# Kernel optimization log

Measured on AMD Instinct MI355X. Metric: run time of the kernel, lower is better.

The kernel has to match this reference:

```python
import jax, jax.numpy as jnp
import numpy as np

NH = 32          # num_attention_heads
LAYER_ID = 3     # -> query_key_layer_scaling_coeff = 4.0
ROPE_BASE = 10000.0


def setup_inputs() -> dict:
    key = jax.random.key(0)
    k1, k2, k3, k4, k5 = jax.random.split(key, 5)
    S, B, H = 2048, 1, 4096
    hidden_states = jax.random.normal(k1, (S, B, H), dtype=jnp.float32)
    position_ids = jnp.broadcast_to(jnp.arange(S, dtype=jnp.int64)[None, :], (B, S))
    # causal mask: True means masked out (torch masked_fill semantics)
    mask = jnp.triu(jnp.ones((S, S), dtype=bool), k=1)[None, None, :, :]
    qkv_w = jax.random.normal(k2, (3 * H, H), dtype=jnp.float32) * 0.02
    qkv_b = jax.random.normal(k3, (3 * H,), dtype=jnp.float32) * 0.02
    dense_w = jax.random.normal(k4, (H, H), dtype=jnp.float32) * 0.02
    dense_b = jax.random.normal(k5, (H,), dtype=jnp.float32) * 0.02
    return {"hidden_states": hidden_states, "position_ids": position_ids, "mask": mask,
            "qkv_w": qkv_w, "qkv_b": qkv_b, "dense_w": dense_w, "dense_b": dense_b}


def _rotate_half(x):
    h = x.shape[-1] // 2
    return jnp.concatenate((-x[..., h:], x[..., :h]), axis=-1)


def reference(hidden_states, position_ids, mask, qkv_w, qkv_b, dense_w, dense_b):
    S, B, H = hidden_states.shape
    nh = NH
    hd = H // nh
    coeff = float(LAYER_ID + 1)

    # fused QKV projection: [S, B, 3H] -> [S, B, nh, 3*hd] -> split
    mixed = hidden_states @ qkv_w.T + qkv_b
    mixed = mixed.reshape(S, B, nh, 3 * hd)
    q, k, v = jnp.split(mixed, 3, axis=-1)  # each [S, B, nh, hd]

    # rotary embedding indexed by position_ids (transposed to [S, B])
    pos = position_ids.T  # [S, B]
    inv_freq = 1.0 / (ROPE_BASE ** (jnp.arange(0, hd, 2, dtype=jnp.float32) / hd))
    freqs = pos.astype(jnp.float32)[..., None] * inv_freq  # [S, B, hd/2]
    emb = jnp.concatenate((freqs, freqs), axis=-1)          # [S, B, hd]
    cos = jnp.cos(emb)[:, :, None, :]                       # [S, B, 1, hd]
    sin = jnp.sin(emb)[:, :, None, :]
    q = q * cos + _rotate_half(q) * sin
    k = k * cos + _rotate_half(k) * sin

    # scaled attention scores with per-layer coefficient
    q = q / (jnp.sqrt(jnp.float32(hd)) * coeff)
    scores = jnp.einsum('sbnh,tbnh->bnst', q, k)            # [B, nh, S, S]
    scores = jnp.where(mask, jnp.float32(-10000.0), scores)
    probs = jax.nn.softmax(scores.astype(jnp.float32) * coeff, axis=-1)
    probs = probs.astype(scores.dtype)

    context = jnp.einsum('bnst,tbnh->sbnh', probs, v).reshape(S, B, H)
    output = context @ dense_w.T + dense_b                  # [S, B, H]
    return output
```

## Files before the change

### kernel.cpp

```cpp
#include <hip/hip_runtime.h>
#include <hip/hip_bf16.h>
#include <cstdint>

#define SQ   2048
#define HIDD 4096
#define NH_  32
#define HD_  128

typedef __attribute__((ext_vector_type(8))) __bf16 bf16x8;
typedef __attribute__((ext_vector_type(4))) float  f32x4;

__device__ __forceinline__ unsigned short f2bf(float f) {
  union { float f; unsigned u; } v; v.f = f;
  return (unsigned short)((v.u + 0x7FFFu + ((v.u >> 16) & 1u)) >> 16);
}
__device__ __forceinline__ float bf2f(unsigned short u) {
  union { unsigned u; float f; } v; v.u = ((unsigned)u) << 16; return v.f;
}
__device__ __forceinline__ void gload16(const void* g, void* l) {
  __builtin_amdgcn_global_load_lds((const __attribute__((address_space(1))) void*)g,
                                   (__attribute__((address_space(3))) void*)l, 16, 0, 0);
}
#define BAR()   asm volatile("s_barrier" ::: "memory")
#define VMC(N)  asm volatile("s_waitcnt vmcnt(" #N ")" ::: "memory")

__global__ __launch_bounds__(256) void k_conv(const float* __restrict__ src,
                                              unsigned short* __restrict__ dst, int n4) {
  int i = blockIdx.x * blockDim.x + threadIdx.x;
  int stride = gridDim.x * blockDim.x;
  for (; i < n4; i += stride) {
    float4 f = ((const float4*)src)[i];
    ushort4 o;
    o.x = f2bf(f.x); o.y = f2bf(f.y); o.z = f2bf(f.z); o.w = f2bf(f.w);
    ((ushort4*)dst)[i] = o;
  }
}

template<int MODE, int BN_>
__global__ __launch_bounds__(256, 2)
void k_gemm3(const unsigned short* __restrict__ A, const unsigned short* __restrict__ B,
             const float* __restrict__ bias, float* __restrict__ outf,
             unsigned short* __restrict__ qb, unsigned short* __restrict__ kb,
             unsigned short* __restrict__ vb, int K) {
  constexpr int NS   = 4 + BN_ / 32;
  constexpr int NF   = BN_ / 64;
  constexpr int BUFB = 16384 + BN_ * 128;
  __shared__ __align__(16) char lds[2 * BUFB];
  const int t = threadIdx.x;
  const int lane = t & 63, wc = t >> 6;
  const int lr = lane & 15, lg = lane >> 4;
  const int gx = gridDim.x;
  const int nwg = gx * gridDim.y;
  const int id = blockIdx.y * gx + blockIdx.x;
  const int cpx = nwg >> 3;
  const int swz = (id & 7) * cpx + (id >> 3);
  const int bm = swz % gx, bn = swz / gx;

  const unsigned short* src[NS];
  int dst[NS];
#pragma unroll
  for (int j = 0; j < NS; ++j) {
    int o = j * 4096 + t * 16;
    dst[j] = o;
    if (o < 16384) {
      int row = o >> 7, colb = o & 127;
      src[j] = A + (size_t)(bm * 128 + row) * K + ((colb ^ ((row & 7) << 4)) >> 1);
    } else {
      int o2 = o - 16384;
      int row = o2 >> 7, colb = o2 & 127;
      src[j] = B + (size_t)(bn * BN_ + row) * K + ((colb ^ ((row & 7) << 4)) >> 1);
    }
  }

  f32x4 acc[8][NF] = {};
  const int nk = K >> 6;
  const int swA = (lr & 7) << 4;

#pragma unroll
  for (int j = 0; j < NS; ++j) gload16(src[j], lds + dst[j]);

  int c = 0;
  for (int kt = 0; kt < nk; ++kt) {
    char* const bufc = lds + c * BUFB;
    char* const bufn = lds + (c ^ 1) * BUFB;
    if (kt + 1 < nk) {
      const int koff = (kt + 1) * 64;
#pragma unroll
      for (int j = 0; j < NS; ++j) gload16(src[j] + koff, bufn + dst[j]);
      if constexpr (NS == 10) VMC(10); else VMC(8);
    } else {
      VMC(0);
    }
    BAR();

    bf16x8 bfr[NF][2];
#pragma unroll
    for (int n = 0; n < NF; ++n) {
      const char* base = bufc + 16384 + (wc * (BN_ / 4) + n * 16 + lr) * 128;
#pragma unroll
      for (int kk = 0; kk < 2; ++kk)
        bfr[n][kk] = *(const bf16x8*)(base + ((kk * 64 + lg * 16) ^ swA));
    }
    __builtin_amdgcn_s_setprio(1);
#pragma unroll
    for (int m = 0; m < 8; ++m) {
      const char* abase = bufc + (m * 16 + lr) * 128;
      bf16x8 a0 = *(const bf16x8*)(abase + ((lg * 16) ^ swA));
      bf16x8 a1 = *(const bf16x8*)(abase + ((64 + lg * 16) ^ swA));
#pragma unroll
      for (int n = 0; n < NF; ++n) {
        acc[m][n] = __builtin_amdgcn_mfma_f32_16x16x32_bf16(a0, bfr[n][0], acc[m][n], 0, 0, 0);
        acc[m][n] = __builtin_amdgcn_mfma_f32_16x16x32_bf16(a1, bfr[n][1], acc[m][n], 0, 0, 0);
      }
    }
    __builtin_amdgcn_s_setprio(0);
    BAR();
    c ^= 1;
  }

#pragma unroll
  for (int m = 0; m < 8; ++m) {
    int row0 = bm * 128 + m * 16 + lg * 4;
#pragma unroll
    for (int n = 0; n < NF; ++n) {
      int col = bn * BN_ + wc * (BN_ / 4) + n * 16 + lr;
      float bv = bias[col];
      if (MODE == 0) {
        int h = col / 384, rem = col - h * 384;
        int sel = rem >> 7, d = rem & 127;
        unsigned short* dstp = sel == 0 ? qb : (sel == 1 ? kb : vb);
#pragma unroll
        for (int r = 0; r < 4; ++r)
          dstp[((size_t)h * SQ + row0 + r) * HD_ + d] = f2bf(acc[m][n][r] + bv);
      } else {
#pragma unroll
        for (int r = 0; r < 4; ++r)
          outf[(size_t)(row0 + r) * HIDD + col] = acc[m][n][r] + bv;
      }
    }
  }
}

__global__ __launch_bounds__(256) void k_rope(unsigned short* __restrict__ q,
                                              unsigned short* __restrict__ k) {
  int idx = blockIdx.x * blockDim.x + threadIdx.x;
  int i = idx & 63;
  int s = (idx >> 6) & (SQ - 1);
  int h = idx >> 17;
  float inv = __expf(-(float)i * (9.210340371976184f / 64.0f));
  float f = (float)s * inv;
  float sn, cs;
  sincosf(f, &sn, &cs);
  size_t base = ((size_t)h * SQ + s) * HD_ + i;
  const float qs = 0.08838834764831845f;
  float q0 = bf2f(q[base]), q1 = bf2f(q[base + 64]);
  q[base]      = f2bf((q0 * cs - q1 * sn) * qs);
  q[base + 64] = f2bf((q1 * cs + q0 * sn) * qs);
  float k0 = bf2f(k[base]), k1 = bf2f(k[base + 64]);
  k[base]      = f2bf(k0 * cs - k1 * sn);
  k[base + 64] = f2bf(k1 * cs + k0 * sn);
}

__global__ __launch_bounds__(256) void k_trans(const unsigned short* __restrict__ v,
                                               unsigned short* __restrict__ vt) {
  __shared__ unsigned short tile[32][33];
  const int h = blockIdx.z;
  const int sb = blockIdx.x * 32, db = blockIdx.y * 32;
  const unsigned short* src = v + (size_t)h * SQ * HD_;
  unsigned short* dst = vt + (size_t)h * HD_ * SQ;
  for (int r = threadIdx.y; r < 32; r += 8)
    tile[r][threadIdx.x] = src[(size_t)(sb + r) * HD_ + db + threadIdx.x];
  __syncthreads();
  for (int r = threadIdx.y; r < 32; r += 8)
    dst[(size_t)(db + r) * SQ + sb + threadIdx.x] = tile[threadIdx.x][r];
}

__global__ __launch_bounds__(256)
void k_attn(const unsigned short* __restrict__ q, const unsigned short* __restrict__ k,
            const unsigned short* __restrict__ vt, unsigned short* __restrict__ ctx) {
  __shared__ __align__(16) unsigned short Ks[64 * 128];
  __shared__ __align__(16) unsigned short Vs[128 * 64];
  __shared__ __align__(16) unsigned short Ps[4][16 * 64];

  const int h = blockIdx.y;
  const int t = threadIdx.x;
  const int lane = t & 63, wv = t >> 6;
  const int lr = lane & 15, lg = lane >> 4;

  const unsigned short* Kg = k + (size_t)h * SQ * HD_;
  const unsigned short* Vg = vt + (size_t)h * HD_ * SQ;
  char* const kl = (char*)Ks;
  char* const vl = (char*)Vs;
  char* const pb = (char*)(Ps[wv]);

  for (int ph = 0; ph < 2; ++ph) {
    const int tph = (ph == 0) ? (int)blockIdx.x : 31 - (int)blockIdx.x;
    const int q0p = tph * 64;
    const int qrow = wv * 16 + lg * 4;

    const unsigned short* Q = q + ((size_t)h * SQ + q0p + wv * 16) * HD_;
    bf16x8 qf[4];
#pragma unroll
    for (int kk = 0; kk < 4; ++kk)
      qf[kk] = *(const bf16x8*)(Q + (size_t)lr * HD_ + kk * 32 + lg * 8);

    f32x4 ot[8] = {};
    float m_r[4], l_r[4];
#pragma unroll
    for (int r = 0; r < 4; ++r) { m_r[r] = -1e30f; l_r[r] = 0.f; }

    const int nkt = tph + 1;
    for (int kt = 0; kt < nkt; ++kt) {
      const int kv0 = kt * 64;
      __syncthreads();
#pragma unroll
      for (int it = 0; it < 4; ++it) {
        int o = it * 4096 + t * 16;
        int krow = o >> 8, kcb = o & 255;
        int kscb = kcb ^ ((krow & 7) << 4);
        gload16(Kg + (size_t)(kv0 + krow) * HD_ + (kscb >> 1), kl + o);
        int vrow = o >> 7, vcb = o & 127;
        int vscb = vcb ^ ((vrow & 7) << 4);
        gload16(Vg + (size_t)vrow * SQ + kv0 + (vscb >> 1), vl + o);
      }
      __syncthreads();

      f32x4 sc[4] = {};
#pragma unroll
      for (int ct = 0; ct < 4; ++ct) {
        int row = ct * 16 + lr;
        const char* kbase = kl + row * 256;
#pragma unroll
        for (int kk = 0; kk < 4; ++kk) {
          bf16x8 kf = *(const bf16x8*)(kbase + ((kk * 64 + lg * 16) ^ ((row & 7) << 4)));
          sc[ct] = __builtin_amdgcn_mfma_f32_16x16x32_bf16(qf[kk], kf, sc[ct], 0, 0, 0);
        }
      }

      if (kt == tph) {
#pragma unroll
        for (int ct = 0; ct < 4; ++ct) {
          int col = ct * 16 + lr;
#pragma unroll
          for (int r = 0; r < 4; ++r)
            if (col > qrow + r) sc[ct][r] = -1e30f;
        }
      }

      float tmax[4];
#pragma unroll
      for (int r = 0; r < 4; ++r)
        tmax[r] = fmaxf(fmaxf(sc[0][r], sc[1][r]), fmaxf(sc[2][r], sc[3][r]));
#pragma unroll
      for (int off = 1; off < 16; off <<= 1)
#pragma unroll
        for (int r = 0; r < 4; ++r) tmax[r] = fmaxf(tmax[r], __shfl_xor(tmax[r], off, 64));

      float scf[4];
#pragma unroll
      for (int r = 0; r < 4; ++r) {
        float mn = fmaxf(m_r[r], tmax[r]);
        scf[r] = __expf(m_r[r] - mn);
        m_r[r] = mn;
      }
      float pr[4][4], rsum[4];
#pragma unroll
      for (int r = 0; r < 4; ++r) rsum[r] = 0.f;
#pragma unroll
      for (int ct = 0; ct < 4; ++ct)
#pragma unroll
        for (int r = 0; r < 4; ++r) {
          pr[ct][r] = __expf(sc[ct][r] - m_r[r]);
          rsum[r] += pr[ct][r];
        }
#pragma unroll
      for (int off = 1; off < 16; off <<= 1)
#pragma unroll
        for (int r = 0; r < 4; ++r) rsum[r] += __shfl_xor(rsum[r], off, 64);
#pragma unroll
      for (int r = 0; r < 4; ++r) l_r[r] = l_r[r] * scf[r] + rsum[r];

#pragma unroll
      for (int dt = 0; dt < 8; ++dt)
#pragma unroll
        for (int r = 0; r < 4; ++r) ot[dt][r] *= scf[r];

#pragma unroll
      for (int ct = 0; ct < 4; ++ct)
#pragma unroll
        for (int r = 0; r < 4; ++r) {
          int row = lg * 4 + r;
          int byte = row * 128 + ((ct * 32 + lr * 2) ^ ((row & 7) << 4));
          *(unsigned short*)(pb + byte) = f2bf(pr[ct][r]);
        }
      bf16x8 pa[2];
#pragma unroll
      for (int k2 = 0; k2 < 2; ++k2)
        pa[k2] = *(const bf16x8*)(pb + lr * 128 + ((k2 * 64 + lg * 16) ^ ((lr & 7) << 4)));

#pragma unroll
      for (int dt = 0; dt < 8; ++dt) {
        int row = dt * 16 + lr;
        const char* vbase = vl + row * 128;
        bf16x8 vf0 = *(const bf16x8*)(vbase + ((lg * 16) ^ ((row & 7) << 4)));
        bf16x8 vf1 = *(const bf16x8*)(vbase + ((64 + lg * 16) ^ ((row & 7) << 4)));
        ot[dt] = __builtin_amdgcn_mfma_f32_16x16x32_bf16(pa[0], vf0, ot[dt], 0, 0, 0);
        ot[dt] = __builtin_amdgcn_mfma_f32_16x16x32_bf16(pa[1], vf1, ot[dt], 0, 0, 0);
      }
    }

    float inv[4];
#pragma unroll
    for (int r = 0; r < 4; ++r) inv[r] = 1.0f / l_r[r];
#pragma unroll
    for (int dt = 0; dt < 8; ++dt)
#pragma unroll
      for (int r = 0; r < 4; ++r)
        ctx[(size_t)(q0p + wv * 16 + lg * 4 + r) * HIDD + h * HD_ + dt * 16 + lr] =
            f2bf(ot[dt][r] * inv[r]);
  }
}

extern "C" void kernel_launch(void* const* d_in, const int* in_sizes, int n_in,
                              void* d_out, int out_size, void* d_ws, size_t ws_size,
                              hipStream_t stream) {
  const float* hidden  = (const float*)d_in[0];
  const float* qkv_w   = (const float*)d_in[3];
  const float* qkv_b   = (const float*)d_in[4];
  const float* dense_w = (const float*)d_in[5];
  const float* dense_b = (const float*)d_in[6];
  float* out = (float*)d_out;

  char* ws = (char*)d_ws;
  unsigned short* wbuf = (unsigned short*)ws;
  unsigned short* hidb = (unsigned short*)(ws + 100663296);
  unsigned short* vtb  = hidb;
  unsigned short* qb   = (unsigned short*)(ws + 117440512);
  unsigned short* kb   = (unsigned short*)(ws + 134217728);
  unsigned short* vb   = (unsigned short*)(ws + 150994944);
  unsigned short* ctx  = (unsigned short*)(ws + 167772160);
  if (ws_size < 184549376ull) return;

  k_conv<<<2048, 256, 0, stream>>>(hidden, hidb, 8388608 / 4);
  k_conv<<<4096, 256, 0, stream>>>(qkv_w, wbuf, 50331648 / 4);
  k_gemm3<0, 192><<<dim3(16, 64), 256, 0, stream>>>(hidb, wbuf, qkv_b, nullptr, qb, kb, vb, 4096);
  k_rope<<<16384, 256, 0, stream>>>(qb, kb);
  k_trans<<<dim3(64, 4, 32), dim3(32, 8), 0, stream>>>(vb, vtb);
  k_attn<<<dim3(16, 32), 256, 0, stream>>>(qb, kb, vtb, ctx);
  k_conv<<<2048, 256, 0, stream>>>(dense_w, wbuf, 16777216 / 4);
  k_gemm3<1, 128><<<dim3(16, 32), 256, 0, stream>>>(ctx, wbuf, dense_b, out, nullptr, nullptr, nullptr, 4096);
}
```

Baseline: 459.4 us.

## Add 128x256 K=32 double-buffered GEMM kernel for QKV projection

Adds a new GEMM kernel that uses 128x256 output tiles with a K-step of 32, a 2-stage LDS double buffer and occupancy hint 3, and uses it for the QKV projection in place of the previous 128x192 multi-stage kernel. Each wave computes a 128x64 slice, so every A fragment read from LDS is reused across four MFMAs. The intent is better operand reuse per LDS read and higher occupancy to hide memory latency. In exchange the pipeline is shallower (only one tile prefetched), there is a barrier every 32-wide K step, and the epilogue still writes scattered bf16 stores.

```diff
diff --git a/kernel.cpp b/kernel.cpp
--- a/kernel.cpp
+++ b/kernel.cpp
@@ -33,6 +33,102 @@
     ushort4 o;
     o.x = f2bf(f.x); o.y = f2bf(f.y); o.z = f2bf(f.z); o.w = f2bf(f.w);
     ((ushort4*)dst)[i] = o;
+  }
+}
+
+template<int MODE>
+__global__ __launch_bounds__(256, 3)
+void k_gemm4(const unsigned short* __restrict__ A, const unsigned short* __restrict__ B,
+             const float* __restrict__ bias, float* __restrict__ outf,
+             unsigned short* __restrict__ qb, unsigned short* __restrict__ kb,
+             unsigned short* __restrict__ vb, int K) {
+  __shared__ __align__(16) char lds[2 * 24576];
+  const int t = threadIdx.x;
+  const int lane = t & 63, wc = t >> 6;
+  const int lr = lane & 15, lg = lane >> 4;
+  const int gx = gridDim.x;
+  const int nwg = gx * gridDim.y;
+  const int id = blockIdx.y * gx + blockIdx.x;
+  const int cpx = nwg >> 3;
+  const int swz = (id & 7) * cpx + (id >> 3);
+  const int bm = swz % gx, bn = swz / gx;
+
+  const unsigned short* src[6];
+  int dst[6];
+#pragma unroll
+  for (int j = 0; j < 6; ++j) {
+    int o = j * 4096 + t * 16;
+    dst[j] = o;
+    if (o < 8192) {
+      int row = o >> 6, colb = o & 63;
+      src[j] = A + (size_t)(bm * 128 + row) * K + ((colb ^ ((row & 3) << 4)) >> 1);
+    } else {
+      int o2 = o - 8192;
+      int row = o2 >> 6, colb = o2 & 63;
+      src[j] = B + (size_t)(bn * 256 + row) * K + ((colb ^ ((row & 3) << 4)) >> 1);
+    }
+  }
+
+  f32x4 acc[8][4] = {};
+  const int nk = K >> 5;
+  const int swF = (lr & 3) << 4;
+
+#pragma unroll
+  for (int j = 0; j < 6; ++j) gload16(src[j], lds + dst[j]);
+
+  int c = 0;
+  for (int kt = 0; kt < nk; ++kt) {
+    char* const bufc = lds + c * 24576;
+    char* const bufn = lds + (c ^ 1) * 24576;
+    if (kt + 1 < nk) {
+      const int koff = (kt + 1) * 32;
+#pragma unroll
+      for (int j = 0; j < 6; ++j) gload16(src[j] + koff, bufn + dst[j]);
+      VMC(6);
+    } else {
+      VMC(0);
+    }
+    BAR();
+
+    bf16x8 bfr[4];
+#pragma unroll
+    for (int n = 0; n < 4; ++n) {
+      int row = wc * 64 + n * 16 + lr;
+      bfr[n] = *(const bf16x8*)(bufc + 8192 + row * 64 + ((lg * 16) ^ swF));
+    }
+    __builtin_amdgcn_s_setprio(1);
+#pragma unroll
+    for (int m = 0; m < 8; ++m) {
+      bf16x8 a0 = *(const bf16x8*)(bufc + (m * 16 + lr) * 64 + ((lg * 16) ^ swF));
+#pragma unroll
+      for (int n = 0; n < 4; ++n)
+        acc[m][n] = __builtin_amdgcn_mfma_f32_16x16x32_bf16(a0, bfr[n], acc[m][n], 0, 0, 0);
+    }
+    __builtin_amdgcn_s_setprio(0);
+    BAR();
+    c ^= 1;
+  }
+
+#pragma unroll
+  for (int m = 0; m < 8; ++m) {
+    int row0 = bm * 128 + m * 16 + lg * 4;
+#pragma unroll
+    for (int n = 0; n < 4; ++n) {
+      int col = bn * 256 + wc * 64 + n * 16 + lr;
+      float bv = bias[col];
+      if (MODE == 0) {
+        int h = col / 384, rem = col - h * 384;
+        int sel = rem >> 7, d = rem & 127;
+        unsigned short* dstp = sel == 0 ? qb : (sel == 1 ? kb : vb);
+#pragma unroll
+        for (int r = 0; r < 4; ++r)
+          dstp[((size_t)h * SQ + row0 + r) * HD_ + d] = f2bf(acc[m][n][r] + bv);
+      } else {
+#pragma unroll
+        for (int r = 0; r < 4; ++r)
+          outf[(size_t)(row0 + r) * HIDD + col] = acc[m][n][r] + bv;
+      }
+    }
   }
 }
 
@@ -343,7 +439,7 @@
 
   k_conv<<<2048, 256, 0, stream>>>(hidden, hidb, 8388608 / 4);
   k_conv<<<4096, 256, 0, stream>>>(qkv_w, wbuf, 50331648 / 4);
-  k_gemm3<0, 192><<<dim3(16, 64), 256, 0, stream>>>(hidb, wbuf, qkv_b, nullptr, qb, kb, vb, 4096);
+  k_gemm4<0><<<dim3(16, 48), 256, 0, stream>>>(hidb, wbuf, qkv_b, nullptr, qb, kb, vb, 4096);
   k_rope<<<16384, 256, 0, stream>>>(qb, kb);
   k_trans<<<dim3(64, 4, 32), dim3(32, 8), 0, stream>>>(vb, vtb);
   k_attn<<<dim3(16, 32), 256, 0, stream>>>(qb, kb, vtb, ctx);
```

New measurement: 479.9 us. 1.04x slower.

## Fuse fp32 weight conversion into GEMM B-operand loads, dropping conversion kernels

Applied to the files above, without the earlier changes.

The GEMM now reads fp32 weights directly from global memory into registers and converts them to bf16 in-kernel, instead of first running separate conversion kernels for the QKV and dense weights. The B operand no longer goes through LDS; only A is staged there, and the loop is manually double-buffered. This removes two full conversion passes (about 64M floats read and written as bf16). In exchange, each GEMM block re-reads fp32 weights (twice the bytes) once per M tile with uncoalesced per-lane row loads, and register pressure rises from the float4 staging buffers.

```diff
diff --git a/kernel.cpp b/kernel.cpp
--- a/kernel.cpp
+++ b/kernel.cpp
@@ -23,6 +23,16 @@
 }
 #define BAR()   asm volatile("s_barrier" ::: "memory")
 #define VMC(N)  asm volatile("s_waitcnt vmcnt(" #N ")" ::: "memory")
+#define MFMA_(a, b, c) __builtin_amdgcn_mfma_f32_16x16x32_bf16(a, b, c, 0, 0, 0)
+
+__device__ __forceinline__ bf16x8 cvt8(float4 a, float4 b) {
+  union { bf16x8 v; __hip_bfloat162 h[4]; } u;
+  u.h[0] = __float22bfloat162_rn(float2{a.x, a.y});
+  u.h[1] = __float22bfloat162_rn(float2{a.z, a.w});
+  u.h[2] = __float22bfloat162_rn(float2{b.x, b.y});
+  u.h[3] = __float22bfloat162_rn(float2{b.z, b.w});
+  return u.v;
+}
 
 __global__ __launch_bounds__(256) void k_conv(const float* __restrict__ src,
                                               unsigned short* __restrict__ dst, int n4) {
@@ -38,14 +48,12 @@
 
 template<int MODE, int BN_>
 __global__ __launch_bounds__(256, 2)
-void k_gemm3(const unsigned short* __restrict__ A, const unsigned short* __restrict__ B,
+void k_gemmF(const unsigned short* __restrict__ A, const float* __restrict__ Bf,
              const float* __restrict__ bias, float* __restrict__ outf,
              unsigned short* __restrict__ qb, unsigned short* __restrict__ kb,
              unsigned short* __restrict__ vb, int K) {
-  constexpr int NS   = 4 + BN_ / 32;
-  constexpr int NF   = BN_ / 64;
-  constexpr int BUFB = 16384 + BN_ * 128;
-  __shared__ __align__(16) char lds[2 * BUFB];
+  constexpr int NF = BN_ / 64;
+  __shared__ __align__(16) char lds[2 * 16384];
   const int t = threadIdx.x;
   const int lane = t & 63, wc = t >> 6;
   const int lr = lane & 15, lg = lane >> 4;
@@ -56,67 +64,81 @@
   const int swz = (id & 7) * cpx + (id >> 3);
   const int bm = swz % gx, bn = swz / gx;
 
-  const unsigned short* src[NS];
-  int dst[NS];
-#pragma unroll
-  for (int j = 0; j < NS; ++j) {
+  const unsigned short* srcA[4];
+  int dstA[4];
+#pragma unroll
+  for (int j = 0; j < 4; ++j) {
     int o = j * 4096 + t * 16;
-    dst[j] = o;
-    if (o < 16384) {
-      int row = o >> 7, colb = o & 127;
-      src[j] = A + (size_t)(bm * 128 + row) * K + ((colb ^ ((row & 7) << 4)) >> 1);
-    } else {
-      int o2 = o - 16384;
-      int row = o2 >> 7, colb = o2 & 127;
-      src[j] = B + (size_t)(bn * BN_ + row) * K + ((colb ^ ((row & 7) << 4)) >> 1);
-    }
-  }
+    int row = o >> 7, colb = o & 127;
+    srcA[j] = A + (size_t)(bm * 128 + row) * K + ((colb ^ ((row & 7) << 4)) >> 1);
+    dstA[j] = o;
+  }
+  const float* bp[NF];
+#pragma unroll
+  for (int n = 0; n < NF; ++n)
+    bp[n] = Bf + (size_t)(bn * BN_ + wc * (BN_ / 4) + n * 16 + lr) * K + lg * 8;
 
   f32x4 acc[8][NF] = {};
   const int nk = K >> 6;
   const int swA = (lr & 7) << 4;
 
-#pragma unroll
-  for (int j = 0; j < NS; ++j) gload16(src[j], lds + dst[j]);
-
-  int c = 0;
-  for (int kt = 0; kt < nk; ++kt) {
-    char* const bufc = lds + c * BUFB;
-    char* const bufn = lds + (c ^ 1) * BUFB;
+  float4 e0[NF][4], e1[NF][4];
+
+  auto gloadA = [&](int kt, char* buf) {
+#pragma unroll
+    for (int j = 0; j < 4; ++j) gload16(srcA[j] + kt * 64, buf + dstA[j]);
+  };
+#define LOADB(e_, kt_)                                                       \
+  {                                                                          \
+    _Pragma("unroll") for (int n = 0; n < NF; ++n)                           \
+        _Pragma("unroll") for (int kk = 0; kk < 2; ++kk)                     \
+            _Pragma("unroll") for (int hh = 0; hh < 2; ++hh)                 \
+        e_[n][kk * 2 + hh] =                                                 \
+            *(const float4*)(bp[n] + (kt_) * 64 + kk * 32 + hh * 4);         \
+  }
+#define COMPUTE(buf_, e_)                                                    \
+  {                                                                          \
+    bf16x8 bfr[NF][2];                                                       \
+    _Pragma("unroll") for (int n = 0; n < NF; ++n) {                         \
+      bfr[n][0] = cvt8(e_[n][0], e_[n][1]);                                  \
+      bfr[n][1] = cvt8(e_[n][2], e_[n][3]);                                  \
+    }                                                                        \
+    __builtin_amdgcn_s_setprio(1);                                           \
+    _Pragma("unroll") for (int m = 0; m < 8; ++m) {                          \
+      const char* abase = (buf_) + (m * 16 + lr) * 128;                      \
+      bf16x8 a0 = *(const bf16x8*)(abase + ((lg * 16) ^ swA));               \
+      bf16x8 a1 = *(const bf16x8*)(abase + ((64 + lg * 16) ^ swA));          \
+      _Pragma("unroll") for (int n = 0; n < NF; ++n) {                       \
+        acc[m][n] = MFMA_(a0, bfr[n][0], acc[m][n]);                         \
+        acc[m][n] = MFMA_(a1, bfr[n][1], acc[m][n]);                         \
+      }                                                                      \
+    }                                                                        \
+    __builtin_amdgcn_s_setprio(0);                                           \
+  }
+
+  gloadA(0, lds);
+  LOADB(e0, 0);
+
+  for (int kt = 0; kt < nk; kt += 2) {
+    BAR();
     if (kt + 1 < nk) {
-      const int koff = (kt + 1) * 64;
-#pragma unroll
-      for (int j = 0; j < NS; ++j) gload16(src[j] + koff, bufn + dst[j]);
-      if constexpr (NS == 10) VMC(10); else VMC(8);
-    } else {
-      VMC(0);
-    }
+      gloadA(kt + 1, lds + 16384);
+      LOADB(e1, kt + 1);
+      if constexpr (NF == 3) VMC(16); else VMC(12);
+    } else { VMC(0); }
     BAR();
-
-    bf16x8 bfr[NF][2];
-#pragma unroll
-    for (int n = 0; n < NF; ++n) {
-      const char* base = bufc + 16384 + (wc * (BN_ / 4) + n * 16 + lr) * 128;
-#pragma unroll
-      for (int kk = 0; kk < 2; ++kk)
-        bfr[n][kk] = *(const bf16x8*)(base + ((kk * 64 + lg * 16) ^ swA));
-    }
-    __builtin_amdgcn_s_setprio(1);
-#pragma unroll
-    for (int m = 0; m < 8; ++m) {
-      const char* abase = bufc + (m * 16 + lr) * 128;
-      bf16x8 a0 = *(const bf16x8*)(abase + ((lg * 16) ^ swA));
-      bf16x8 a1 = *(const bf16x8*)(abase + ((64 + lg * 16) ^ swA));
-#pragma unroll
-      for (int n = 0; n < NF; ++n) {
-        acc[m][n] = __builtin_amdgcn_mfma_f32_16x16x32_bf16(a0, bfr[n][0], acc[m][n], 0, 0, 0);
-        acc[m][n] = __builtin_amdgcn_mfma_f32_16x16x32_bf16(a1, bfr[n][1], acc[m][n], 0, 0, 0);
-      }
-    }
-    __builtin_amdgcn_s_setprio(0);
+    COMPUTE(lds, e0);
     BAR();
-    c ^= 1;
-  }
+    if (kt + 2 < nk) {
+      gloadA(kt + 2, lds);
+      LOADB(e0, kt + 2);
+      if constexpr (NF == 3) VMC(16); else VMC(12);
+    } else { VMC(0); }
+    BAR();
+    COMPUTE(lds + 16384, e1);
+  }
+#undef LOADB
+#undef COMPUTE
 
 #pragma unroll
   for (int m = 0; m < 8; ++m) {
@@ -233,7 +255,7 @@
 #pragma unroll
         for (int kk = 0; kk < 4; ++kk) {
           bf16x8 kf = *(const bf16x8*)(kbase + ((kk * 64 + lg * 16) ^ ((row & 7) << 4)));
-          sc[ct] = __builtin_amdgcn_mfma_f32_16x16x32_bf16(qf[kk], kf, sc[ct], 0, 0, 0);
+          sc[ct] = MFMA_(qf[kk], kf, sc[ct]);
         }
       }
 
@@ -304,8 +326,8 @@
         const char* vbase = vl + row * 128;
         bf16x8 vf0 = *(const bf16x8*)(vbase + ((lg * 16) ^ ((row & 7) << 4)));
         bf16x8 vf1 = *(const bf16x8*)(vbase + ((64 + lg * 16) ^ ((row & 7) << 4)));
-        ot[dt] = __builtin_amdgcn_mfma_f32_16x16x32_bf16(pa[0], vf0, ot[dt], 0, 0, 0);
-        ot[dt] = __builtin_amdgcn_mfma_f32_16x16x32_bf16(pa[1], vf1, ot[dt], 0, 0, 0);
+        ot[dt] = MFMA_(pa[0], vf0, ot[dt]);
+        ot[dt] = MFMA_(pa[1], vf1, ot[dt]);
       }
     }
 
@@ -332,7 +354,6 @@
   float* out = (float*)d_out;
 
   char* ws = (char*)d_ws;
-  unsigned short* wbuf = (unsigned short*)ws;
   unsigned short* hidb = (unsigned short*)(ws + 100663296);
   unsigned short* vtb  = hidb;
   unsigned short* qb   = (unsigned short*)(ws + 117440512);
@@ -342,11 +363,9 @@
   if (ws_size < 184549376ull) return;
 
   k_conv<<<2048, 256, 0, stream>>>(hidden, hidb, 8388608 / 4);
-  k_conv<<<4096, 256, 0, stream>>>(qkv_w, wbuf, 50331648 / 4);
-  k_gemm3<0, 192><<<dim3(16, 64), 256, 0, stream>>>(hidb, wbuf, qkv_b, nullptr, qb, kb, vb, 4096);
+  k_gemmF<0, 192><<<dim3(16, 64), 256, 0, stream>>>(hidb, qkv_w, qkv_b, nullptr, qb, kb, vb, 4096);
   k_rope<<<16384, 256, 0, stream>>>(qb, kb);
   k_trans<<<dim3(64, 4, 32), dim3(32, 8), 0, stream>>>(vb, vtb);
   k_attn<<<dim3(16, 32), 256, 0, stream>>>(qb, kb, vtb, ctx);
-  k_conv<<<2048, 256, 0, stream>>>(dense_w, wbuf, 16777216 / 4);
-  k_gemm3<1, 128><<<dim3(16, 32), 256, 0, stream>>>(ctx, wbuf, dense_b, out, nullptr, nullptr, nullptr, 4096);
-}
+  k_gemmF<1, 128><<<dim3(16, 32), 256, 0, stream>>>(ctx, dense_w, dense_b, out, nullptr, nullptr, nullptr, 4096);
+}
```

Result: slower. 698.1 us (+52.0%).
